# Kernel optimization log

Hardware: AMD Instinct MI355X
Metric: run time of the kernel (lower is better)

Reference implementation:

```python
import jax, jax.numpy as jnp
import numpy as np

N_NODES = 50000
N_EDGES = 800000
D_IN, D_HID, D_OUT = 128, 128, 64
BN_EPS = 1e-5


def gcn_conv(x, W, b, src, dst, ew, n):
    # PyG GCNConv: out[i] = sum_j norm_ij * (x @ W)[j] + b, with self-loops added
    xw = x @ W                                   # [N, D_out]
    loop = jnp.arange(n)
    s = jnp.concatenate([src, loop])             # add self-loops (weight 1)
    d = jnp.concatenate([dst, loop])
    w = jnp.concatenate([ew, jnp.ones((n,), x.dtype)])
    deg = jax.ops.segment_sum(w, d, num_segments=n)
    dinv = jnp.where(deg > 0, jax.lax.rsqrt(deg), 0.0)
    norm = dinv[s] * w * dinv[d]                 # symmetric normalization
    msg = xw[s] * norm[:, None]                  # gather + scale  [E+N, D_out]
    return jax.ops.segment_sum(msg, d, num_segments=n) + b


def setup_inputs() -> dict:
    key = jax.random.key(0)
    ks = jax.random.split(key, 12)
    x = jax.random.normal(ks[0], (N_NODES, D_IN), dtype=jnp.float32)
    edge_index = jax.random.randint(ks[1], (2, N_EDGES), 0, N_NODES, dtype=jnp.int64)
    edge_weight = jax.random.uniform(ks[2], (N_EDGES,), dtype=jnp.float32)
    W1 = jax.random.normal(ks[3], (D_IN, D_HID), dtype=jnp.float32) * 0.05
    b1 = jnp.zeros((D_HID,), jnp.float32)
    gamma = jnp.ones((D_HID,), jnp.float32)
    beta = jnp.zeros((D_HID,), jnp.float32)
    running_mean = jax.random.normal(ks[4], (D_HID,), dtype=jnp.float32) * 0.1
    running_var = jax.random.uniform(ks[5], (D_HID,), dtype=jnp.float32) + 0.5
    W2 = jax.random.normal(ks[6], (D_HID, D_OUT), dtype=jnp.float32) * 0.05
    b2 = jnp.zeros((D_OUT,), jnp.float32)
    return {"x": x, "edge_index": edge_index, "edge_weight": edge_weight,
            "W1": W1, "b1": b1, "gamma": gamma, "beta": beta,
            "running_mean": running_mean, "running_var": running_var,
            "W2": W2, "b2": b2}


def reference(x, edge_index, edge_weight, W1, b1, gamma, beta,
              running_mean, running_var, W2, b2):
    src, dst = edge_index[0], edge_index[1]
    n = x.shape[0]
    h = gcn_conv(x, W1, b1, src, dst, edge_weight, n)
    # BatchNorm1d in eval mode (running stats); dropout inactive in eval
    h = (h - running_mean) * jax.lax.rsqrt(running_var + BN_EPS) * gamma + beta
    h = jax.nn.relu(h)
    out = gcn_conv(h, W2, b2, src, dst, edge_weight, n)
    return out
```

## Files before the change

### kernel.cpp

```cpp
#include <hip/hip_runtime.h>
#include <hip/hip_fp16.h>

#define BN_EPS 1e-5f
#define PAD 64

static __device__ __forceinline__ unsigned short f2bf(float f) {
    unsigned u = __float_as_uint(f);
    u += 0x7FFF + ((u >> 16) & 1);
    return (unsigned short)(u >> 16);
}
static __device__ __forceinline__ float bf2f(unsigned short b) {
    return __uint_as_float((unsigned)b << 16);
}
static __device__ __forceinline__ unsigned pk(int s, float w) {
    return ((unsigned)s << 16) | (unsigned)__half_as_ushort(__float2half_rn(w));
}
static __device__ __forceinline__ float pw(unsigned e) {
    return __half2float(__ushort_as_half((unsigned short)(e & 0xFFFFu)));
}

__global__ __launch_bounds__(256) void k_fused(const int* __restrict__ src, const int* __restrict__ dst,
                                               const float* __restrict__ ew,
                                               int* cnt, unsigned* __restrict__ pad, int e, int gfill, int stride,
                                               const float* __restrict__ A, const float* __restrict__ W,
                                               unsigned short* __restrict__ C, int n,
                                               const float* __restrict__ b1, const float* __restrict__ gamma,
                                               const float* __restrict__ beta, const float* __restrict__ mean,
                                               const float* __restrict__ var,
                                               float* __restrict__ bnscale, float* __restrict__ bnshift,
                                               const float* __restrict__ W2, unsigned short* __restrict__ w2bf) {
    __shared__ float WsQ[32 * 128];
    __shared__ float AsT[128 * 32];
    int tid = threadIdx.x;
    int b = (int)blockIdx.x;
    int gGemm = (n + 31) / 32;

    bool isFill = ((b % stride) == 0) && (b / stride < gfill);
    if (isFill) {
        int i0 = ((b / stride) * 256 + tid) * 8;
        if (i0 + 7 < e) {
            int4   s0 = *(const int4*)(src + i0), s1 = *(const int4*)(src + i0 + 4);
            int4   d0 = *(const int4*)(dst + i0), d1 = *(const int4*)(dst + i0 + 4);
            float4 w0 = *(const float4*)(ew + i0), w1 = *(const float4*)(ew + i0 + 4);
            int p0 = atomicAdd(&cnt[d0.x], 1);
            int p1 = atomicAdd(&cnt[d0.y], 1);
            int p2 = atomicAdd(&cnt[d0.z], 1);
            int p3 = atomicAdd(&cnt[d0.w], 1);
            int p4 = atomicAdd(&cnt[d1.x], 1);
            int p5 = atomicAdd(&cnt[d1.y], 1);
            int p6 = atomicAdd(&cnt[d1.z], 1);
            int p7 = atomicAdd(&cnt[d1.w], 1);
            if (p0 < PAD) pad[(size_t)d0.x * PAD + p0] = pk(s0.x, w0.x);
            if (p1 < PAD) pad[(size_t)d0.y * PAD + p1] = pk(s0.y, w0.y);
            if (p2 < PAD) pad[(size_t)d0.z * PAD + p2] = pk(s0.z, w0.z);
            if (p3 < PAD) pad[(size_t)d0.w * PAD + p3] = pk(s0.w, w0.w);
            if (p4 < PAD) pad[(size_t)d1.x * PAD + p4] = pk(s1.x, w1.x);
            if (p5 < PAD) pad[(size_t)d1.y * PAD + p5] = pk(s1.y, w1.y);
            if (p6 < PAD) pad[(size_t)d1.z * PAD + p6] = pk(s1.z, w1.z);
            if (p7 < PAD) pad[(size_t)d1.w * PAD + p7] = pk(s1.w, w1.w);
        } else {
            for (int i = i0; i < e; ++i) {
                int d = dst[i];
                int p = atomicAdd(&cnt[d], 1);
                if (p < PAD) pad[(size_t)d * PAD + p] = pk(src[i], ew[i]);
            }
        }
        return;
    }

    int fillsBefore = (b == 0) ? 0 : min(gfill, (b - 1) / stride + 1);
    int g = b - fillsBefore;
    if (g == gGemm) {
        if (tid < 128) {
            float sc = gamma[tid] * rsqrtf(var[tid] + BN_EPS);
            bnscale[tid] = sc;
            bnshift[tid] = (b1[tid] - mean[tid]) * sc + beta[tid];
        }
        const float4* W4 = (const float4*)W2;
        ushort4* O = (ushort4*)w2bf;
        #pragma unroll
        for (int q = 0; q < 8; ++q) {
            float4 v = W4[q * 256 + tid];
            O[q * 256 + tid] = make_ushort4(f2bf(v.x), f2bf(v.y), f2bf(v.z), f2bf(v.w));
        }
        return;
    }

    int row0 = g * 32;
    {
        int lr = tid & 31, kq = tid >> 5;
        int gr = row0 + lr; if (gr > n - 1) gr = n - 1;
        const float4* A4 = (const float4*)(A + (size_t)gr * 128);
        #pragma unroll
        for (int j = 0; j < 4; ++j) {
            float4 v = A4[kq * 4 + j];
            int k = kq * 16 + j * 4;
            AsT[(k + 0) * 32 + lr] = v.x;
            AsT[(k + 1) * 32 + lr] = v.y;
            AsT[(k + 2) * 32 + lr] = v.z;
            AsT[(k + 3) * 32 + lr] = v.w;
        }
    }
    int cg_ = tid & 31, rg = tid >> 5;
    float4 acc0 = make_float4(0, 0, 0, 0), acc1 = acc0, acc2 = acc0, acc3 = acc0;
    const float4* W4 = (const float4*)W;
    float4* WsQ4 = (float4*)WsQ;
    const float4* AsT4 = (const float4*)AsT;
    for (int ph = 0; ph < 4; ++ph) {
        __syncthreads();
        #pragma unroll
        for (int j = 0; j < 4; ++j)
            WsQ4[j * 256 + tid] = W4[ph * 1024 + j * 256 + tid];
        __syncthreads();
        #pragma unroll 16
        for (int kk = 0; kk < 32; ++kk) {
            float4 w = WsQ4[kk * 32 + cg_];
            float4 a = AsT4[(ph * 32 + kk) * 8 + rg];
            acc0.x += a.x * w.x; acc0.y += a.x * w.y; acc0.z += a.x * w.z; acc0.w += a.x * w.w;
            acc1.x += a.y * w.x; acc1.y += a.y * w.y; acc1.z += a.y * w.z; acc1.w += a.y * w.w;
            acc2.x += a.z * w.x; acc2.y += a.z * w.y; acc2.z += a.z * w.z; acc2.w += a.z * w.w;
            acc3.x += a.w * w.x; acc3.y += a.w * w.y; acc3.z += a.w * w.z; acc3.w += a.w * w.w;
        }
    }
    ushort4* C4 = (ushort4*)C;
    int r = row0 + rg * 4;
    if (r + 0 < n) C4[(size_t)(r + 0) * 32 + cg_] = make_ushort4(f2bf(acc0.x), f2bf(acc0.y), f2bf(acc0.z), f2bf(acc0.w));
    if (r + 1 < n) C4[(size_t)(r + 1) * 32 + cg_] = make_ushort4(f2bf(acc1.x), f2bf(acc1.y), f2bf(acc1.z), f2bf(acc1.w));
    if (r + 2 < n) C4[(size_t)(r + 2) * 32 + cg_] = make_ushort4(f2bf(acc2.x), f2bf(acc2.y), f2bf(acc2.z), f2bf(acc2.w));
    if (r + 3 < n) C4[(size_t)(r + 3) * 32 + cg_] = make_ushort4(f2bf(acc3.x), f2bf(acc3.y), f2bf(acc3.z), f2bf(acc3.w));
}

__global__ __launch_bounds__(256) void k_deg(const int* __restrict__ cnt, const unsigned* __restrict__ pad,
                                             float* __restrict__ dinv, int n) {
    int i = blockIdx.x * 256 + threadIdx.x;
    if (i < n) {
        int c = min(cnt[i], PAD);
        size_t base = (size_t)i * PAD;
        const uint4* row = (const uint4*)(pad + base);
        float s = 1.0f;
        int p = 0;
        for (; p + 3 < c; p += 4) {
            uint4 v = row[p >> 2];
            s += pw(v.x) + pw(v.y) + pw(v.z) + pw(v.w);
        }
        for (; p < c; ++p) s += pw(pad[base + p]);
        dinv[i] = rsqrtf(s);
    }
}

__global__ __launch_bounds__(256) void k_ag12(const unsigned short* __restrict__ xw, const int* __restrict__ cnt,
                                              const unsigned* __restrict__ pad,
                                              const float* __restrict__ dinv,
                                              const float* __restrict__ scale, const float* __restrict__ shift,
                                              const unsigned short* __restrict__ w2bf,
                                              unsigned short* __restrict__ hw2, int n) {
    __shared__ unsigned short W2s[128 * 64];
    int tid = threadIdx.x;
    {
        const uint4* s4 = (const uint4*)w2bf;
        uint4* d4 = (uint4*)W2s;
        #pragma unroll
        for (int q = 0; q < 4; ++q) d4[q * 256 + tid] = s4[q * 256 + tid];
    }
    __syncthreads();

    int g = tid >> 5;
    int lc = tid & 31;
    int node = blockIdx.x * 8 + g;
    if (node >= n) return;

    unsigned hu0, hu1;
    {
        const ushort4* X4 = (const ushort4*)xw;
        float di = dinv[node];
        int c = min(cnt[node], PAD);
        size_t base = (size_t)node * PAD;
        ushort4 q0 = X4[(size_t)node * 32 + lc];
        float4 acc0 = make_float4(bf2f(q0.x) * di, bf2f(q0.y) * di, bf2f(q0.z) * di, bf2f(q0.w) * di);
        float4 acc1 = make_float4(0, 0, 0, 0);
        float4 acc2 = make_float4(0, 0, 0, 0);
        float4 acc3 = make_float4(0, 0, 0, 0);
        int p = 0;
        for (; p + 3 < c; p += 4) {
            uint4 ee = *(const uint4*)(pad + base + p);
            float w0 = pw(ee.x) * dinv[ee.x >> 16];
            float w1 = pw(ee.y) * dinv[ee.y >> 16];
            float w2 = pw(ee.z) * dinv[ee.z >> 16];
            float w3 = pw(ee.w) * dinv[ee.w >> 16];
            ushort4 a = X4[(size_t)(ee.x >> 16) * 32 + lc];
            ushort4 b = X4[(size_t)(ee.y >> 16) * 32 + lc];
            ushort4 gg = X4[(size_t)(ee.z >> 16) * 32 + lc];
            ushort4 d = X4[(size_t)(ee.w >> 16) * 32 + lc];
            acc0.x += w0 * bf2f(a.x); acc0.y += w0 * bf2f(a.y); acc0.z += w0 * bf2f(a.z); acc0.w += w0 * bf2f(a.w);
            acc1.x += w1 * bf2f(b.x); acc1.y += w1 * bf2f(b.y); acc1.z += w1 * bf2f(b.z); acc1.w += w1 * bf2f(b.w);
            acc2.x += w2 * bf2f(gg.x); acc2.y += w2 * bf2f(gg.y); acc2.z += w2 * bf2f(gg.z); acc2.w += w2 * bf2f(gg.w);
            acc3.x += w3 * bf2f(d.x); acc3.y += w3 * bf2f(d.y); acc3.z += w3 * bf2f(d.z); acc3.w += w3 * bf2f(d.w);
        }
        for (; p < c; ++p) {
            unsigned e0 = pad[base + p];
            float w0 = pw(e0) * dinv[e0 >> 16];
            ushort4 a = X4[(size_t)(e0 >> 16) * 32 + lc];
            acc0.x += w0 * bf2f(a.x); acc0.y += w0 * bf2f(a.y); acc0.z += w0 * bf2f(a.z); acc0.w += w0 * bf2f(a.w);
        }
        acc0.x = (acc0.x + acc1.x + acc2.x + acc3.x) * di;
        acc0.y = (acc0.y + acc1.y + acc2.y + acc3.y) * di;
        acc0.z = (acc0.z + acc1.z + acc2.z + acc3.z) * di;
        acc0.w = (acc0.w + acc1.w + acc2.w + acc3.w) * di;
        float4 Sc = ((const float4*)scale)[lc];
        float4 Sh = ((const float4*)shift)[lc];
        unsigned short r0 = f2bf(fmaxf(acc0.x * Sc.x + Sh.x, 0.0f));
        unsigned short r1 = f2bf(fmaxf(acc0.y * Sc.y + Sh.y, 0.0f));
        unsigned short r2 = f2bf(fmaxf(acc0.z * Sc.z + Sh.z, 0.0f));
        unsigned short r3 = f2bf(fmaxf(acc0.w * Sc.w + Sh.w, 0.0f));
        hu0 = ((unsigned)r1 << 16) | (unsigned)r0;
        hu1 = ((unsigned)r3 << 16) | (unsigned)r2;
    }

    float a0 = 0.0f, a1 = 0.0f;
    const unsigned* W2u = (const unsigned*)W2s;
    #pragma unroll 8
    for (int k = 0; k < 32; ++k) {
        unsigned p0 = (unsigned)__shfl((int)hu0, k, 32);
        unsigned p1 = (unsigned)__shfl((int)hu1, k, 32);
        float h0 = bf2f((unsigned short)(p0 & 0xFFFFu));
        float h1 = bf2f((unsigned short)(p0 >> 16));
        float h2 = bf2f((unsigned short)(p1 & 0xFFFFu));
        float h3 = bf2f((unsigned short)(p1 >> 16));
        unsigned w0u = W2u[(4 * k + 0) * 32 + lc];
        unsigned w1u = W2u[(4 * k + 1) * 32 + lc];
        unsigned w2u = W2u[(4 * k + 2) * 32 + lc];
        unsigned w3u = W2u[(4 * k + 3) * 32 + lc];
        a0 += h0 * bf2f((unsigned short)(w0u & 0xFFFFu));
        a1 += h0 * bf2f((unsigned short)(w0u >> 16));
        a0 += h1 * bf2f((unsigned short)(w1u & 0xFFFFu));
        a1 += h1 * bf2f((unsigned short)(w1u >> 16));
        a0 += h2 * bf2f((unsigned short)(w2u & 0xFFFFu));
        a1 += h2 * bf2f((unsigned short)(w2u >> 16));
        a0 += h3 * bf2f((unsigned short)(w3u & 0xFFFFu));
        a1 += h3 * bf2f((unsigned short)(w3u >> 16));
    }
    unsigned outp = ((unsigned)f2bf(a1) << 16) | (unsigned)f2bf(a0);
    ((unsigned*)hw2)[(size_t)node * 32 + lc] = outp;
}

__global__ __launch_bounds__(256) void k_agg2(const unsigned short* __restrict__ hw, const int* __restrict__ cnt,
                                              const unsigned* __restrict__ pad,
                                              const float* __restrict__ dinv,
                                              const float* __restrict__ b2, float* __restrict__ out, int n) {
    int node = blockIdx.x * 16 + (threadIdx.x >> 4);
    if (node >= n) return;
    int lc = threadIdx.x & 15;
    const ushort4* X4 = (const ushort4*)hw;
    float di = dinv[node];
    int c = min(cnt[node], PAD);
    size_t base = (size_t)node * PAD;
    ushort4 q0 = X4[(size_t)node * 16 + lc];
    float4 acc0 = make_float4(bf2f(q0.x) * di, bf2f(q0.y) * di, bf2f(q0.z) * di, bf2f(q0.w) * di);
    float4 acc1 = make_float4(0, 0, 0, 0);
    float4 acc2 = make_float4(0, 0, 0, 0);
    float4 acc3 = make_float4(0, 0, 0, 0);
    int p = 0;
    for (; p + 3 < c; p += 4) {
        uint4 ee = *(const uint4*)(pad + base + p);
        float w0 = pw(ee.x) * dinv[ee.x >> 16];
        float w1 = pw(ee.y) * dinv[ee.y >> 16];
        float w2 = pw(ee.z) * dinv[ee.z >> 16];
        float w3 = pw(ee.w) * dinv[ee.w >> 16];
        ushort4 a = X4[(size_t)(ee.x >> 16) * 16 + lc];
        ushort4 b = X4[(size_t)(ee.y >> 16) * 16 + lc];
        ushort4 g = X4[(size_t)(ee.z >> 16) * 16 + lc];
        ushort4 d = X4[(size_t)(ee.w >> 16) * 16 + lc];
        acc0.x += w0 * bf2f(a.x); acc0.y += w0 * bf2f(a.y); acc0.z += w0 * bf2f(a.z); acc0.w += w0 * bf2f(a.w);
        acc1.x += w1 * bf2f(b.x); acc1.y += w1 * bf2f(b.y); acc1.z += w1 * bf2f(b.z); acc1.w += w1 * bf2f(b.w);
        acc2.x += w2 * bf2f(g.x); acc2.y += w2 * bf2f(g.y); acc2.z += w2 * bf2f(g.z); acc2.w += w2 * bf2f(g.w);
        acc3.x += w3 * bf2f(d.x); acc3.y += w3 * bf2f(d.y); acc3.z += w3 * bf2f(d.z); acc3.w += w3 * bf2f(d.w);
    }
    for (; p < c; ++p) {
        unsigned e0 = pad[base + p];
        float w0 = pw(e0) * dinv[e0 >> 16];
        ushort4 a = X4[(size_t)(e0 >> 16) * 16 + lc];
        acc0.x += w0 * bf2f(a.x); acc0.y += w0 * bf2f(a.y); acc0.z += w0 * bf2f(a.z); acc0.w += w0 * bf2f(a.w);
    }
    float4 B = ((const float4*)b2)[lc];
    acc0.x = (acc0.x + acc1.x + acc2.x + acc3.x) * di + B.x;
    acc0.y = (acc0.y + acc1.y + acc2.y + acc3.y) * di + B.y;
    acc0.z = (acc0.z + acc1.z + acc2.z + acc3.z) * di + B.z;
    acc0.w = (acc0.w + acc1.w + acc2.w + acc3.w) * di + B.w;
    ((float4*)out)[(size_t)node * 16 + lc] = acc0;
}


extern "C" void kernel_launch(void* const* d_in, const int* in_sizes, int n_in,
                              void* d_out, int out_size, void* d_ws, size_t ws_size,
                              hipStream_t stream) {
    const float* x     = (const float*)d_in[0];
    const int*   ei    = (const int*)d_in[1];
    const float* ew    = (const float*)d_in[2];
    const float* W1    = (const float*)d_in[3];
    const float* b1    = (const float*)d_in[4];
    const float* gamma = (const float*)d_in[5];
    const float* beta  = (const float*)d_in[6];
    const float* rmean = (const float*)d_in[7];
    const float* rvar  = (const float*)d_in[8];
    const float* W2    = (const float*)d_in[9];
    const float* b2    = (const float*)d_in[10];
    float* out = (float*)d_out;

    int N = in_sizes[0] / 128;
    int E = in_sizes[2];
    const int* src = ei;
    const int* dst = ei + E;

    char* p = (char*)d_ws;
    auto carve = [&](size_t bytes) { char* q = p; p += (bytes + 255) & ~(size_t)255; return (void*)q; };
    int*      cnt     = (int*)     carve(sizeof(int) * (size_t)N);
    unsigned* pad     = (unsigned*)carve(sizeof(unsigned) * (size_t)N * PAD);
    float*    dinv    = (float*)   carve(sizeof(float) * (size_t)N);
    float*    bnscale = (float*)   carve(sizeof(float) * 128);
    float*    bnshift = (float*)   carve(sizeof(float) * 128);
    unsigned short* w2bf = (unsigned short*)carve(sizeof(unsigned short) * 128 * 64);
    unsigned short* xw1  = (unsigned short*)carve(sizeof(unsigned short) * (size_t)N * 128);
    unsigned short* hw2  = (unsigned short*)carve(sizeof(unsigned short) * (size_t)N * 64);

    int gN    = (N + 255) / 256;
    int gFill = (E + 2047) / 2048;
    int gGemm = (N + 31) / 32;
    int T     = gFill + gGemm + 1;
    int S     = T / gFill;
    if (S < 2) S = 2;

    hipMemsetAsync(cnt, 0, sizeof(int) * (size_t)N, stream);
    k_fused <<<T, 256, 0, stream>>>(src, dst, ew, cnt, pad, E, gFill, S,
                                    x, W1, xw1, N,
                                    b1, gamma, beta, rmean, rvar, bnscale, bnshift,
                                    W2, w2bf);
    k_deg   <<<gN, 256, 0, stream>>>(cnt, pad, dinv, N);
    k_ag12  <<<(N + 7) / 8, 256, 0, stream>>>(xw1, cnt, pad, dinv, bnscale, bnshift, w2bf, hw2, N);
    k_agg2  <<<(N + 15) / 16, 256, 0, stream>>>(hw2, cnt, pad, dinv, b2, out, N);
}
```

Measured before the change: 209.7 us.

## Compute first-layer GEMM with bf16 MFMA instead of scalar FP32 FMAs

The x@W1 part of the fused kernel now uses 16x16x32 bf16 MFMA instructions. Each block converts W1 to bf16 in shared memory in an MFMA-friendly layout and processes 64 rows instead of 32, with A operands converted from fp32 on the fly. This replaces the FP32 LDS-tiled outer-product loop and aims to cut the GEMM blocks' compute time. In exchange, every block re-converts all of W1, inputs are rounded to bf16 before the multiply, and output stores become scalar 2-byte writes.

```diff
diff --git a/kernel.cpp b/kernel.cpp
--- a/kernel.cpp
+++ b/kernel.cpp
@@ -3,6 +3,9 @@
 
 #define BN_EPS 1e-5f
 #define PAD 64
+
+typedef __attribute__((ext_vector_type(8))) short short8;
+typedef __attribute__((ext_vector_type(4))) float f32x4;
 
 static __device__ __forceinline__ unsigned short f2bf(float f) {
     unsigned u = __float_as_uint(f);
@@ -29,11 +32,10 @@
                                                const float* __restrict__ var,
                                                float* __restrict__ bnscale, float* __restrict__ bnshift,
                                                const float* __restrict__ W2, unsigned short* __restrict__ w2bf) {
-    __shared__ float WsQ[32 * 128];
-    __shared__ float AsT[128 * 32];
+    __shared__ unsigned short W1s[16384];
     int tid = threadIdx.x;
     int b = (int)blockIdx.x;
-    int gGemm = (n + 31) / 32;
+    int gGemm = (n + 63) / 64;
 
     bool isFill = ((b % stride) == 0) && (b / stride < gfill);
     if (isFill) {
@@ -86,48 +88,73 @@
         return;
     }
 
-    int row0 = g * 32;
+    int row0 = g * 64;
+
     {
-        int lr = tid & 31, kq = tid >> 5;
-        int gr = row0 + lr; if (gr > n - 1) gr = n - 1;
-        const float4* A4 = (const float4*)(A + (size_t)gr * 128);
+        int k  = tid >> 1;
+        int c0 = (tid & 1) * 64;
+        int kk = k >> 5, lg = (k >> 3) & 3, ii = k & 7;
+        int tbase = kk * 4096 + lg * 128 + ii;
+        const float4* Wr = (const float4*)(W + (size_t)k * 128 + c0);
         #pragma unroll
-        for (int j = 0; j < 4; ++j) {
-            float4 v = A4[kq * 4 + j];
-            int k = kq * 16 + j * 4;
-            AsT[(k + 0) * 32 + lr] = v.x;
-            AsT[(k + 1) * 32 + lr] = v.y;
-            AsT[(k + 2) * 32 + lr] = v.z;
-            AsT[(k + 3) * 32 + lr] = v.w;
-        }
-    }
-    int cg_ = tid & 31, rg = tid >> 5;
-    float4 acc0 = make_float4(0, 0, 0, 0), acc1 = acc0, acc2 = acc0, acc3 = acc0;
-    const float4* W4 = (const float4*)W;
-    float4* WsQ4 = (float4*)WsQ;
-    const float4* AsT4 = (const float4*)AsT;
-    for (int ph = 0; ph < 4; ++ph) {
-        __syncthreads();
-        #pragma unroll
-        for (int j = 0; j < 4; ++j)
-            WsQ4[j * 256 + tid] = W4[ph * 1024 + j * 256 + tid];
-        __syncthreads();
-        #pragma unroll 16
-        for (int kk = 0; kk < 32; ++kk) {
-            float4 w = WsQ4[kk * 32 + cg_];
-            float4 a = AsT4[(ph * 32 + kk) * 8 + rg];
-            acc0.x += a.x * w.x; acc0.y += a.x * w.y; acc0.z += a.x * w.z; acc0.w += a.x * w.w;
-            acc1.x += a.y * w.x; acc1.y += a.y * w.y; acc1.z += a.y * w.z; acc1.w += a.y * w.w;
-            acc2.x += a.z * w.x; acc2.y += a.z * w.y; acc2.z += a.z * w.z; acc2.w += a.z * w.w;
-            acc3.x += a.w * w.x; acc3.y += a.w * w.y; acc3.z += a.w * w.z; acc3.w += a.w * w.w;
-        }
-    }
-    ushort4* C4 = (ushort4*)C;
-    int r = row0 + rg * 4;
-    if (r + 0 < n) C4[(size_t)(r + 0) * 32 + cg_] = make_ushort4(f2bf(acc0.x), f2bf(acc0.y), f2bf(acc0.z), f2bf(acc0.w));
-    if (r + 1 < n) C4[(size_t)(r + 1) * 32 + cg_] = make_ushort4(f2bf(acc1.x), f2bf(acc1.y), f2bf(acc1.z), f2bf(acc1.w));
-    if (r + 2 < n) C4[(size_t)(r + 2) * 32 + cg_] = make_ushort4(f2bf(acc2.x), f2bf(acc2.y), f2bf(acc2.z), f2bf(acc2.w));
-    if (r + 3 < n) C4[(size_t)(r + 3) * 32 + cg_] = make_ushort4(f2bf(acc3.x), f2bf(acc3.y), f2bf(acc3.z), f2bf(acc3.w));
+        for (int j = 0; j < 16; ++j) {
+            float4 v = Wr[j];
+            int n0 = c0 + j * 4;
+            W1s[tbase + ((n0 + 0) >> 4) * 512 + ((n0 + 0) & 15) * 8] = f2bf(v.x);
+            W1s[tbase + ((n0 + 1) >> 4) * 512 + ((n0 + 1) & 15) * 8] = f2bf(v.y);
+            W1s[tbase + ((n0 + 2) >> 4) * 512 + ((n0 + 2) & 15) * 8] = f2bf(v.z);
+            W1s[tbase + ((n0 + 3) >> 4) * 512 + ((n0 + 3) & 15) * 8] = f2bf(v.w);
+        }
+    }
+    __syncthreads();
+
+    int w = tid >> 6, lane = tid & 63;
+    int arow = row0 + w * 16 + (lane & 15);
+    if (arow > n - 1) arow = n - 1;
+    const float* xrow = A + (size_t)arow * 128 + ((lane >> 4) * 8);
+    const unsigned short* Wl = W1s + (size_t)lane * 8;
+
+    f32x4 z = {0.f, 0.f, 0.f, 0.f};
+    f32x4 acc0 = z, acc1 = z, acc2 = z, acc3 = z, acc4 = z, acc5 = z, acc6 = z, acc7 = z;
+
+    #pragma unroll
+    for (int kk = 0; kk < 4; ++kk) {
+        float4 v0 = *(const float4*)(xrow + kk * 32);
+        float4 v1 = *(const float4*)(xrow + kk * 32 + 4);
+        short8 a;
+        a[0] = (short)f2bf(v0.x); a[1] = (short)f2bf(v0.y);
+        a[2] = (short)f2bf(v0.z); a[3] = (short)f2bf(v0.w);
+        a[4] = (short)f2bf(v1.x); a[5] = (short)f2bf(v1.y);
+        a[6] = (short)f2bf(v1.z); a[7] = (short)f2bf(v1.w);
+        const unsigned short* Wk = Wl + kk * 4096;
+        short8 b0 = *(const short8*)(Wk);
+        short8 b1 = *(const short8*)(Wk + 512);
+        short8 b2 = *(const short8*)(Wk + 1024);
+        short8 b3 = *(const short8*)(Wk + 1536);
+        short8 b4 = *(const short8*)(Wk + 2048);
+        short8 b5 = *(const short8*)(Wk + 2560);
+        short8 b6 = *(const short8*)(Wk + 3072);
+        short8 b7 = *(const short8*)(Wk + 3584);
+        acc0 = __builtin_amdgcn_mfma_f32_16x16x32_bf16(a, b0, acc0, 0, 0, 0);
+        acc1 = __builtin_amdgcn_mfma_f32_16x16x32_bf16(a, b1, acc1, 0, 0, 0);
+        acc2 = __builtin_amdgcn_mfma_f32_16x16x32_bf16(a, b2, acc2, 0, 0, 0);
+        acc3 = __builtin_amdgcn_mfma_f32_16x16x32_bf16(a, b3, acc3, 0, 0, 0);
+        acc4 = __builtin_amdgcn_mfma_f32_16x16x32_bf16(a, b4, acc4, 0, 0, 0);
+        acc5 = __builtin_amdgcn_mfma_f32_16x16x32_bf16(a, b5, acc5, 0, 0, 0);
+        acc6 = __builtin_amdgcn_mfma_f32_16x16x32_bf16(a, b6, acc6, 0, 0, 0);
+        acc7 = __builtin_amdgcn_mfma_f32_16x16x32_bf16(a, b7, acc7, 0, 0, 0);
+    }
+
+    int rw = row0 + w * 16 + ((lane >> 4) << 2);
+    int cb = lane & 15;
+    #define STORE_NT(av, nt)                                                              \
+        if (rw + 0 < n) C[(size_t)(rw + 0) * 128 + (nt)*16 + cb] = f2bf(av[0]);           \
+        if (rw + 1 < n) C[(size_t)(rw + 1) * 128 + (nt)*16 + cb] = f2bf(av[1]);           \
+        if (rw + 2 < n) C[(size_t)(rw + 2) * 128 + (nt)*16 + cb] = f2bf(av[2]);           \
+        if (rw + 3 < n) C[(size_t)(rw + 3) * 128 + (nt)*16 + cb] = f2bf(av[3]);
+    STORE_NT(acc0, 0) STORE_NT(acc1, 1) STORE_NT(acc2, 2) STORE_NT(acc3, 3)
+    STORE_NT(acc4, 4) STORE_NT(acc5, 5) STORE_NT(acc6, 6) STORE_NT(acc7, 7)
+    #undef STORE_NT
 }
 
 __global__ __launch_bounds__(256) void k_deg(const int* __restrict__ cnt, const unsigned* __restrict__ pad,
@@ -324,7 +351,7 @@
 
     int gN    = (N + 255) / 256;
     int gFill = (E + 2047) / 2048;
-    int gGemm = (N + 31) / 32;
+    int gGemm = (N + 63) / 64;
     int T     = gFill + gGemm + 1;
     int S     = T / gFill;
     if (S < 2) S = 2;
```

Measured after the change: 214.5 us. 2.3% more time.
